# Performance work log

Hardware: AMD Instinct MI355X
Metric: run time of the kernel (lower is better)

Reference implementation:

```python
import jax, jax.numpy as jnp
import numpy as np

D_MODEL, H, DK, DV = 1024, 16, 64, 64
B, NQ, NK = 4, 1024, 1024
LN_EPS = 1e-5


def setup_inputs() -> dict:
    key = jax.random.key(0)
    ks = jax.random.split(key, 16)
    xavier = lambda k, i, o: jax.random.uniform(k, (i, o), jnp.float32,
                                                -np.sqrt(6.0 / (i + o)), np.sqrt(6.0 / (i + o)))
    return {
        "queries": jax.random.normal(ks[0], (B, NQ, D_MODEL), jnp.float32),
        "keys": jax.random.normal(ks[1], (B, NK, D_MODEL), jnp.float32),
        "values": jax.random.normal(ks[2], (B, NK, D_MODEL), jnp.float32),
        "geometry": jax.random.uniform(ks[3], (B, H, NQ, NK), jnp.float32),
        "attention_mask": jax.random.bernoulli(ks[4], 0.1, (B, H, NQ, NK)),
        "Wq": xavier(ks[5], D_MODEL, H * DK), "bq": jnp.zeros((H * DK,), jnp.float32),
        "Wk": xavier(ks[6], D_MODEL, H * DK), "bk": jnp.zeros((H * DK,), jnp.float32),
        "Wv": xavier(ks[7], D_MODEL, H * DV), "bv": jnp.zeros((H * DV,), jnp.float32),
        "Wo": xavier(ks[8], H * DV, D_MODEL), "bo": jnp.zeros((D_MODEL,), jnp.float32),
        "ln_gamma": jnp.ones((D_MODEL,), jnp.float32),
        "ln_beta": jnp.zeros((D_MODEL,), jnp.float32),
    }


def reference(queries, keys, values, geometry, attention_mask,
              Wq, bq, Wk, bk, Wv, bv, Wo, bo, ln_gamma, ln_beta):
    b, nq, _ = queries.shape
    nk = keys.shape[1]
    # QKV projections -> (b, h, n, d)
    q = (queries @ Wq + bq).reshape(b, nq, H, DK).transpose(0, 2, 1, 3)
    k = (keys @ Wk + bk).reshape(b, nk, H, DK).transpose(0, 2, 1, 3)
    v = (values @ Wv + bv).reshape(b, nk, H, DV).transpose(0, 2, 1, 3)
    att = jnp.einsum('bhqd,bhkd->bhqk', q, k) / np.sqrt(DK).astype(np.float32)
    att = jnp.where(attention_mask, -jnp.inf, att)
    # inline geometry log-bias before softmax
    w = jnp.log(jnp.clip(geometry, 1e-6)) + att
    w = jax.nn.softmax(w, axis=-1)  # dropout is identity in eval
    out = jnp.einsum('bhqk,bhkd->bqhd', w, v).reshape(b, nq, H * DV)
    out = out @ Wo + bo
    # residual + LayerNorm
    x = queries + out  # dropout identity in eval
    mu = jnp.mean(x, axis=-1, keepdims=True)
    var = jnp.mean((x - mu) ** 2, axis=-1, keepdims=True)
    return (x - mu) * jax.lax.rsqrt(var + LN_EPS) * ln_gamma + ln_beta
```

## Files before the change

### kernel.cpp

```cpp
#include <hip/hip_runtime.h>
#include <hip/hip_bf16.h>

typedef unsigned short u16;
typedef unsigned long long u64;
typedef __bf16 bf16x8 __attribute__((ext_vector_type(8)));
typedef float f32x4 __attribute__((ext_vector_type(4)));
typedef float f32x2 __attribute__((ext_vector_type(2)));

#define AS1 __attribute__((address_space(1)))
#define AS3 __attribute__((address_space(3)))
#define GLL16(gp, lp) __builtin_amdgcn_global_load_lds((AS1 const unsigned int*)(gp), (AS3 unsigned int*)(lp), 16, 0, 0)

__device__ __forceinline__ u16 f2bf(float f) {
    unsigned u = __builtin_bit_cast(unsigned, f);
    unsigned r = u + 0x7FFFu + ((u >> 16) & 1u);
    return (u16)(r >> 16);
}

__global__ void detect_kernel(const unsigned char* __restrict__ m, int* __restrict__ flag) {
    __shared__ int cnt1;
    __shared__ int big;
    if (threadIdx.x == 0) { cnt1 = 0; big = 0; }
    __syncthreads();
    int c1 = 0, bg = 0;
    for (int i = threadIdx.x; i < 16384; i += 256) {
        unsigned char v = m[i];
        if (v) {
            if ((i & 3) == 1) c1++;
            if (v > 1) bg++;
        }
    }
    atomicAdd(&cnt1, c1);
    atomicAdd(&big, bg);
    __syncthreads();
    if (threadIdx.x == 0) {
        int f;
        if (big == 0) f = cnt1 ? 0 : 1;
        else          f = cnt1 ? 3 : 2;
        *flag = f;
    }
}

#define MN_LOOP(PRED)                                                     \
    for (int row = wave; row < 65536; row += nw) {                        \
        size_t base = (size_t)row * 1024;                                 \
        u64 myw = 0;                                                      \
        _Pragma("unroll")                                                 \
        for (int kb = 0; kb < 16; ++kb) {                                 \
            size_t gi = base + kb * 64 + lane;                            \
            bool p = (PRED);                                              \
            u64 w = __ballot(p);                                          \
            if (lane == kb) myw = w;                                      \
        }                                                                 \
        if (lane < 16) MB[(size_t)row * 16 + lane] = myw;                 \
    }

__global__ __launch_bounds__(256) void masknorm_kernel(const void* __restrict__ mp,
                                                       const int* __restrict__ flagp,
                                                       u64* __restrict__ MB) {
    const int flag = *flagp;
    const int lane = threadIdx.x & 63;
    const int wave = blockIdx.x * 4 + (threadIdx.x >> 6);
    const int nw = gridDim.x * 4;
    if (flag == 0) {
        const unsigned char* m8 = (const unsigned char*)mp;
        MN_LOOP(m8[gi] != 0)
    } else if (flag == 1) {
        const int* m32 = (const int*)mp;
        MN_LOOP(m32[gi] != 0)
    } else if (flag == 2) {
        const unsigned* mf = (const unsigned*)mp;
        MN_LOOP((mf[gi] << 1) != 0)
    } else {
        const u16* mb = (const u16*)mp;
        MN_LOOP((mb[gi] & 0x7FFF) != 0)
    }
}

__global__ void cast3_kernel(const float* __restrict__ q, const float* __restrict__ k,
                             const float* __restrict__ v, u16* __restrict__ xq,
                             u16* __restrict__ xk, u16* __restrict__ xv) {
    const int n4 = 4 * 1024 * 1024 / 4;
    int stride = gridDim.x * blockDim.x;
    for (int i = blockIdx.x * blockDim.x + threadIdx.x; i < n4; i += stride) {
        float4 a = ((const float4*)q)[i];
        float4 b = ((const float4*)k)[i];
        float4 c = ((const float4*)v)[i];
        ((ushort4*)xq)[i] = make_ushort4(f2bf(a.x), f2bf(a.y), f2bf(a.z), f2bf(a.w));
        ((ushort4*)xk)[i] = make_ushort4(f2bf(b.x), f2bf(b.y), f2bf(b.z), f2bf(b.w));
        ((ushort4*)xv)[i] = make_ushort4(f2bf(c.x), f2bf(c.y), f2bf(c.z), f2bf(c.w));
    }
}

__global__ __launch_bounds__(256) void wtrans_kernel(
    const float* __restrict__ W0, const float* __restrict__ W1,
    const float* __restrict__ W2, const float* __restrict__ W3,
    u16* __restrict__ T0, u16* __restrict__ T1, u16* __restrict__ T2, u16* __restrict__ T3) {
    const float* W = (blockIdx.z == 0) ? W0 : (blockIdx.z == 1) ? W1 : (blockIdx.z == 2) ? W2 : W3;
    u16* T = (blockIdx.z == 0) ? T0 : (blockIdx.z == 1) ? T1 : (blockIdx.z == 2) ? T2 : T3;
    __shared__ float t[64][65];
    const int n0 = blockIdx.x * 64, k0 = blockIdx.y * 64;
    const int tx = threadIdx.x, ty = threadIdx.y;
    for (int j = ty; j < 64; j += 4) t[j][tx] = W[(size_t)(k0 + j) * 1024 + n0 + tx];
    __syncthreads();
    for (int j = ty; j < 64; j += 4) T[(size_t)(n0 + j) * 1024 + k0 + tx] = f2bf(t[tx][j]);
}

__device__ __forceinline__ void gemm_core(const u16* __restrict__ A, const u16* __restrict__ Bt,
                                          u16* sA, u16* sB, f32x4 (&acc)[4][4],
                                          int tid, int bm, int bn) {
    const int lane = tid & 63, wid = tid >> 6;
    const int wr = wid >> 1, wc = wid & 1;
    const int l15 = lane & 15, l4 = lane >> 4;
    const int srow = tid >> 2, sslot = tid & 3;
    const int soff = (sslot ^ ((srow >> 1) & 3)) * 8;
    const u16* aSrc = A + (size_t)(bm * 128 + srow) * 1024 + soff;
    const u16* bSrc = Bt + (size_t)(bn * 128 + srow) * 1024 + soff;
    u16* const dA0 = sA + wid * 512;
    u16* const dA1 = sA + 2048 + wid * 512;
    u16* const dB0 = sB + wid * 512;
    u16* const dB1 = sB + 2048 + wid * 512;

#define GSTAGE(BUF, T)                                                  \
    do {                                                                \
        GLL16(aSrc + (T) * 32, dA0 + (BUF) * 4096);                     \
        GLL16(aSrc + 65536 + (T) * 32, dA1 + (BUF) * 4096);             \
        GLL16(bSrc + (T) * 32, dB0 + (BUF) * 4096);                     \
        GLL16(bSrc + 65536 + (T) * 32, dB1 + (BUF) * 4096);             \
    } while (0)

#define GCOMPUTE(BUF)                                                             \
    do {                                                                          \
        bf16x8 af[4], bfv[4];                                                     \
        _Pragma("unroll")                                                         \
        for (int m = 0; m < 4; ++m) {                                             \
            const int rr = wr * 64 + m * 16 + l15;                                \
            af[m] = *(const bf16x8*)(sA + (BUF) * 4096 + rr * 32 +                \
                                     ((l4 ^ ((rr >> 1) & 3)) * 8));               \
        }                                                                         \
        _Pragma("unroll")                                                         \
        for (int n = 0; n < 4; ++n) {                                             \
            const int rr = wc * 64 + n * 16 + l15;                                \
            bfv[n] = *(const bf16x8*)(sB + (BUF) * 4096 + rr * 32 +               \
                                      ((l4 ^ ((rr >> 1) & 3)) * 8));              \
        }                                                                         \
        _Pragma("unroll")                                                         \
        for (int m = 0; m < 4; ++m)                                               \
            _Pragma("unroll")                                                     \
            for (int n = 0; n < 4; ++n)                                           \
                acc[m][n] = __builtin_amdgcn_mfma_f32_16x16x32_bf16(af[m], bfv[n], acc[m][n], 0, 0, 0); \
    } while (0)

#define GBODY(T, BUF, NBUF, WSTR)                                       \
    do {                                                                \
        if ((T) + 2 < 32) {                                             \
            GSTAGE(NBUF, (T) + 2);                                      \
            __builtin_amdgcn_sched_barrier(0);                          \
        }                                                               \
        GCOMPUTE(BUF);                                                  \
        if ((T) + 1 < 32) {                                             \
            asm volatile(WSTR ::: "memory");                            \
            __builtin_amdgcn_sched_barrier(0);                          \
            __builtin_amdgcn_s_barrier();                               \
            __builtin_amdgcn_sched_barrier(0);                          \
        }                                                               \
    } while (0)

    GSTAGE(0, 0);
    GSTAGE(1, 1);
    __builtin_amdgcn_sched_barrier(0);
    asm volatile("s_waitcnt vmcnt(4)" ::: "memory");
    __builtin_amdgcn_sched_barrier(0);
    __builtin_amdgcn_s_barrier();
    __builtin_amdgcn_sched_barrier(0);

    for (int it = 0; it < 10; ++it) {
        const int t0 = it * 3;
        GBODY(t0 + 0, 0, 2, "s_waitcnt vmcnt(4)");
        GBODY(t0 + 1, 1, 0, "s_waitcnt vmcnt(4)");
        GBODY(t0 + 2, 2, 1, "s_waitcnt vmcnt(4)");
    }
    GBODY(30, 0, 2, "s_waitcnt vmcnt(0)");
    GBODY(31, 1, 0, "s_waitcnt vmcnt(0)");
#undef GBODY
#undef GCOMPUTE
#undef GSTAGE
}

__global__ __launch_bounds__(256, 3) void qkv_gemm(
    const u16* __restrict__ XQ, const u16* __restrict__ XK, const u16* __restrict__ XV,
    const u16* __restrict__ WQT, const u16* __restrict__ WKT, const u16* __restrict__ WVT,
    const float* __restrict__ bq, const float* __restrict__ bk, const float* __restrict__ bv,
    u16* __restrict__ QS, u16* __restrict__ KS, u16* __restrict__ VT) {
    __shared__ __align__(16) u16 smem[24576];
    const int z = blockIdx.z;
    const u16* A  = (z == 0) ? XQ : (z == 1) ? XK : XV;
    const u16* Bt = (z == 0) ? WQT : (z == 1) ? WKT : WVT;
    const float* bias = (z == 0) ? bq : (z == 1) ? bk : bv;
    const int tid = threadIdx.x, lane = tid & 63, wid = tid >> 6;
    const int bm = blockIdx.y, bn = blockIdx.x;
    const int wr = wid >> 1, wc = wid & 1;
    const int l15 = lane & 15, l4 = lane >> 4;

    f32x4 acc[4][4] = {};
    gemm_core(A, Bt, smem, smem + 12288, acc, tid, bm, bn);

    if (z == 2) {
        __syncthreads();
        u16* tl = smem;
#pragma unroll
        for (int n = 0; n < 4; ++n) {
            const int cl = wc * 64 + n * 16 + l15;
            const float bv_ = bias[bn * 128 + cl];
#pragma unroll
            for (int m = 0; m < 4; ++m)
#pragma unroll
                for (int j = 0; j < 4; ++j) {
                    const int rl = wr * 64 + m * 16 + l4 * 4 + j;
                    tl[cl * 132 + rl] = f2bf(acc[m][n][j] + bv_);
                }
        }
        __syncthreads();
        const int bb = bm >> 3, k0 = (bm & 7) * 128;
#pragma unroll
        for (int i = 0; i < 8; ++i) {
            const int idx = i * 256 + tid;
            const int row = idx >> 4, col16 = idx & 15;
            const int cg = bn * 128 + row;
            const int hh = cg >> 6, dd = cg & 63;
            bf16x8 v = *(const bf16x8*)(tl + row * 132 + col16 * 8);
            *(bf16x8*)(VT + ((size_t)((bb * 16 + hh) * 64 + dd)) * 1024 + k0 + col16 * 8) = v;
        }
    } else {
        u16* outp = (z == 0) ? QS : KS;
        const float scale = (z == 0) ? 0.125f : 1.0f;
#pragma unroll
        for (int n = 0; n < 4; ++n) {
            const int c = bn * 128 + wc * 64 + n * 16 + l15;
            const float bv_ = bias[c];
#pragma unroll
            for (int m = 0; m < 4; ++m)
#pragma unroll
                for (int j = 0; j < 4; ++j) {
                    const int r = bm * 128 + wr * 64 + m * 16 + l4 * 4 + j;
                    outp[(size_t)r * 1024 + c] = f2bf((acc[m][n][j] + bv_) * scale);
                }
        }
    }
}

__global__ __launch_bounds__(256, 3) void gemm_out(
    const u16* __restrict__ A, const u16* __restrict__ Bt, const float* __restrict__ bias,
    float* __restrict__ outp, const float* __restrict__ resid) {
    __shared__ __align__(16) u16 smem[24576];
    const int tid = threadIdx.x, lane = tid & 63, wid = tid >> 6;
    const int bm = blockIdx.y, bn = blockIdx.x;
    const int wr = wid >> 1, wc = wid & 1;
    const int l15 = lane & 15, l4 = lane >> 4;

    f32x4 acc[4][4] = {};
    gemm_core(A, Bt, smem, smem + 12288, acc, tid, bm, bn);

#pragma unroll
    for (int n = 0; n < 4; ++n) {
        const int c = bn * 128 + wc * 64 + n * 16 + l15;
        const float bv = bias[c];
#pragma unroll
        for (int m = 0; m < 4; ++m)
#pragma unroll
            for (int j = 0; j < 4; ++j) {
                const int r = bm * 128 + wr * 64 + m * 16 + l4 * 4 + j;
                outp[(size_t)r * 1024 + c] = acc[m][n][j] + bv + resid[(size_t)r * 1024 + c];
            }
    }
}

__global__ __launch_bounds__(256, 4) void attn_kernel(
    const u16* __restrict__ Qs, const u16* __restrict__ Ks, const u16* __restrict__ Vt,
    const float* __restrict__ geom, const u64* __restrict__ MBw,
    u16* __restrict__ AO) {
    __shared__ __align__(16) u16 lds[14336];

    const int g = blockIdx.x;
    const int tt = (g & 7) * 128 + (g >> 3);
    const int qb = tt & 15;
    const int bhid = tt >> 4;
    const int b = bhid >> 4, h = bhid & 15;
    const int q0 = qb * 64;

    const int tid = threadIdx.x, lane = tid & 63, wid = tid >> 6;
    const int l15 = lane & 15, l4 = lane >> 4;
    const int qrow = q0 + wid * 16;
    const size_t bh = (size_t)bhid;

    const u16* qp = Qs + (size_t)(b * 1024 + qrow + l15) * 1024 + h * 64 + l4 * 8;
    bf16x8 aq0 = *(const bf16x8*)qp;
    bf16x8 aq1 = *(const bf16x8*)(qp + 32);

    const int kr = tid >> 3, ks = tid & 7;
    const int kgr = (kr & 15) * 2 + (kr >> 4);
    const u16* ksrc = Ks + (size_t)(b * 1024 + kgr) * 1024 + h * 64 + ((ks ^ ((kr >> 1) & 7)) * 8);
    const int vr = tid >> 2, vs = tid & 3;
    const u16* vsrc = Vt + (bh * 64 + vr) * 1024 + ((vs ^ ((vr >> 1) & 3)) * 8);
    u16* const KD0 = lds + 0    + wid * 512;
    u16* const KD1 = lds + 2048 + wid * 512;
    u16* const KD2 = lds + 4096 + wid * 512;
    u16* const VD0 = lds + 6144 + 0    + wid * 512;
    u16* const VD1 = lds + 6144 + 2048 + wid * 512;
    u16* const VD2 = lds + 6144 + 4096 + wid * 512;
    u16* const pw  = lds + 12288 + wid * 512;

    const float* gbase = geom + (bh * 1024 + qrow + l4 * 4) * 1024 + l15 * 2;
    const unsigned* mb32 = (const unsigned*)(MBw + (bh * 1024 + qrow + l4 * 4) * 16);

    f32x4 o[4] = {};
    float m_run[4], l_run[4];
#pragma unroll
    for (int j = 0; j < 4; ++j) { m_run[j] = -1e30f; l_run[j] = 0.f; }

    f32x2 gpA[4], gpB[4];
    unsigned mkA[4], mkB[4];

    GLL16(ksrc, KD0);
    GLL16(vsrc, VD0);
    GLL16(ksrc + 32768, KD1);
    GLL16(vsrc + 32, VD1);
    __builtin_amdgcn_sched_barrier(0);
#pragma unroll
    for (int j = 0; j < 4; ++j) {
        gpA[j] = *(const f32x2*)(gbase + j * 1024);
        mkA[j] = mb32[j * 32];
    }
    __builtin_amdgcn_sched_barrier(0);
    asm volatile("s_waitcnt vmcnt(10)" ::: "memory");
    __builtin_amdgcn_sched_barrier(0);
    __builtin_amdgcn_s_barrier();
    __builtin_amdgcn_sched_barrier(0);

#define BODY(T, GC, GN, MC, MN, KBC, VBC, KDN, VDN, WSTR)                                \
    do {                                                                                 \
        if ((T) + 2 < 32) {                                                              \
            GLL16(ksrc + (size_t)((T) + 2) * 32768, KDN);                                \
            GLL16(vsrc + ((T) + 2) * 32, VDN);                                           \
            __builtin_amdgcn_sched_barrier(0);                                           \
        }                                                                                \
        if ((T) + 1 < 32) {                                                              \
            _Pragma("unroll")                                                            \
            for (int j = 0; j < 4; ++j) {                                                \
                GN[j] = *(const f32x2*)(gbase + j * 1024 + ((T) + 1) * 32);              \
                MN[j] = mb32[j * 32 + (T) + 1];                                          \
            }                                                                            \
            __builtin_amdgcn_sched_barrier(0);                                           \
        }                                                                                \
        f32x4 s0, s1;                                                                    \
        __builtin_amdgcn_s_setprio(1);                                                   \
        {                                                                                \
            const int rr = l15, swz = (rr >> 1) & 7;                                     \
            bf16x8 k0 = *(const bf16x8*)((KBC) + rr * 64 + ((l4 ^ swz) * 8));            \
            bf16x8 k1 = *(const bf16x8*)((KBC) + rr * 64 + (((4 + l4) ^ swz) * 8));      \
            f32x4 z = {};                                                                \
            z = __builtin_amdgcn_mfma_f32_16x16x32_bf16(aq0, k0, z, 0, 0, 0);            \
            s0 = __builtin_amdgcn_mfma_f32_16x16x32_bf16(aq1, k1, z, 0, 0, 0);           \
        }                                                                                \
        {                                                                                \
            const int rr = 16 + l15, swz = (rr >> 1) & 7;                                \
            bf16x8 k0 = *(const bf16x8*)((KBC) + rr * 64 + ((l4 ^ swz) * 8));            \
            bf16x8 k1 = *(const bf16x8*)((KBC) + rr * 64 + (((4 + l4) ^ swz) * 8));      \
            f32x4 z = {};                                                                \
            z = __builtin_amdgcn_mfma_f32_16x16x32_bf16(aq0, k0, z, 0, 0, 0);            \
            s1 = __builtin_amdgcn_mfma_f32_16x16x32_bf16(aq1, k1, z, 0, 0, 0);           \
        }                                                                                \
        __builtin_amdgcn_s_setprio(0);                                                   \
        float sclv[4];                                                                   \
        _Pragma("unroll")                                                                \
        for (int j = 0; j < 4; ++j) {                                                    \
            float a0 = s0[j], a1 = s1[j];                                                \
            float mt = fmaxf(a0, a1);                                                    \
            mt = fmaxf(mt, __shfl_xor(mt, 1, 16));                                       \
            mt = fmaxf(mt, __shfl_xor(mt, 2, 16));                                       \
            mt = fmaxf(mt, __shfl_xor(mt, 4, 16));                                       \
            mt = fmaxf(mt, __shfl_xor(mt, 8, 16));                                       \
            float mn = fmaxf(m_run[j], mt);                                              \
            float scl = __expf(m_run[j] - mn);                                           \
            m_run[j] = mn;                                                               \
            unsigned mb2 = (MC[j] >> (l15 * 2)) & 3u;                                    \
            f32x2 gv = GC[j];                                                            \
            float p0 = (mb2 & 1u) ? 0.f : __expf(a0 - mn) * fmaxf(gv[0], 1e-6f);         \
            float p1 = (mb2 & 2u) ? 0.f : __expf(a1 - mn) * fmaxf(gv[1], 1e-6f);         \
            float rs = p0 + p1;                                                          \
            rs += __shfl_xor(rs, 1, 16);                                                 \
            rs += __shfl_xor(rs, 2, 16);                                                 \
            rs += __shfl_xor(rs, 4, 16);                                                 \
            rs += __shfl_xor(rs, 8, 16);                                                 \
            l_run[j] = l_run[j] * scl + rs;                                              \
            sclv[j] = scl;                                                               \
            const int row = l4 * 4 + j;                                                  \
            const int slot4 = (l15 & 3) | ((((l15 >> 2) ^ l4) & 3) << 2);                \
            unsigned pk = (unsigned)f2bf(p0) | ((unsigned)f2bf(p1) << 16);               \
            *(unsigned*)(pw + row * 32 + slot4 * 2) = pk;                                \
        }                                                                                \
        _Pragma("unroll")                                                                \
        for (int df = 0; df < 4; ++df) {                                                 \
            f32x4 tv = o[df];                                                            \
            _Pragma("unroll")                                                            \
            for (int j = 0; j < 4; ++j) tv[j] *= sclv[j];                                \
            o[df] = tv;                                                                  \
        }                                                                                \
        {                                                                                \
            const int blk = (l4 ^ (l15 >> 2)) & 3;                                       \
            bf16x8 pa = *(const bf16x8*)(pw + l15 * 32 + blk * 8);                       \
            __builtin_amdgcn_s_setprio(1);                                               \
            _Pragma("unroll")                                                            \
            for (int df = 0; df < 4; ++df) {                                             \
                const int rr = df * 16 + l15, vswz = (rr >> 1) & 3;                      \
                bf16x8 v0 = *(const bf16x8*)((VBC) + rr * 32 + ((l4 ^ vswz) * 8));       \
                o[df] = __builtin_amdgcn_mfma_f32_16x16x32_bf16(pa, v0, o[df], 0, 0, 0); \
            }                                                                            \
            __builtin_amdgcn_s_setprio(0);                                               \
        }                                                                                \
        if ((T) + 1 < 32) {                                                              \
            asm volatile(WSTR ::: "memory");                                             \
            __builtin_amdgcn_sched_barrier(0);                                           \
            __builtin_amdgcn_s_barrier();                                                \
            __builtin_amdgcn_sched_barrier(0);                                           \
        }                                                                                \
    } while (0)

    for (int it = 0; it < 5; ++it) {
        const int t0 = it * 6;
        BODY(t0 + 0, gpA, gpB, mkA, mkB, (lds + 0),    (lds + 6144),        KD2, VD2, "s_waitcnt vmcnt(10)");
        BODY(t0 + 1, gpB, gpA, mkB, mkA, (lds + 2048), (lds + 6144 + 2048), KD0, VD0, "s_waitcnt vmcnt(10)");
        BODY(t0 + 2, gpA, gpB, mkA, mkB, (lds + 4096), (lds + 6144 + 4096), KD1, VD1, "s_waitcnt vmcnt(10)");
        BODY(t0 + 3, gpB, gpA, mkB, mkA, (lds + 0),    (lds + 6144),        KD2, VD2, "s_waitcnt vmcnt(10)");
        BODY(t0 + 4, gpA, gpB, mkA, mkB, (lds + 2048), (lds + 6144 + 2048), KD0, VD0, "s_waitcnt vmcnt(10)");
        BODY(t0 + 5, gpB, gpA, mkB, mkA, (lds + 4096), (lds + 6144 + 4096), KD1, VD1, "s_waitcnt vmcnt(10)");
    }
    BODY(30, gpA, gpB, mkA, mkB, (lds + 0),    (lds + 6144),        KD2, VD2, "s_waitcnt vmcnt(8)");
    BODY(31, gpB, gpA, mkB, mkA, (lds + 2048), (lds + 6144 + 2048), KD0, VD0, "s_waitcnt vmcnt(8)");
#undef BODY

    float inv[4];
#pragma unroll
    for (int j = 0; j < 4; ++j) inv[j] = 1.0f / l_run[j];
#pragma unroll
    for (int p = 0; p < 2; ++p) {
#pragma unroll
        for (int df2 = 0; df2 < 2; ++df2) {
            const int df = p * 2 + df2;
#pragma unroll
            for (int j = 0; j < 4; ++j)
                pw[(l4 * 4 + j) * 32 + df2 * 16 + l15] = f2bf(o[df][j] * inv[j]);
        }
        const int er = lane >> 2, ec = lane & 3;
        bf16x8 val = *(const bf16x8*)(pw + er * 32 + ec * 8);
        *(bf16x8*)(AO + (size_t)(b * 1024 + qrow + er) * 1024 + h * 64 + p * 32 + ec * 8) = val;
    }
}

__global__ __launch_bounds__(256) void ln_kernel(const float* __restrict__ Y,
                                                 const float* __restrict__ gamma,
                                                 const float* __restrict__ beta,
                                                 float* __restrict__ out) {
    __shared__ float red[8];
    const int r = blockIdx.x, tid = threadIdx.x, lane = tid & 63, wid = tid >> 6;
    float4 v = ((const float4*)(Y + (size_t)r * 1024))[tid];
    float s = v.x + v.y + v.z + v.w;
    float q = v.x * v.x + v.y * v.y + v.z * v.z + v.w * v.w;
    for (int d = 1; d < 64; d <<= 1) {
        s += __shfl_xor(s, d, 64);
        q += __shfl_xor(q, d, 64);
    }
    if (lane == 0) { red[wid] = s; red[4 + wid] = q; }
    __syncthreads();
    float ts = red[0] + red[1] + red[2] + red[3];
    float tq = red[4] + red[5] + red[6] + red[7];
    float mu = ts * (1.f / 1024.f);
    float var = tq * (1.f / 1024.f) - mu * mu;
    float rstd = rsqrtf(var + 1e-5f);
    float4 gg = ((const float4*)gamma)[tid];
    float4 be = ((const float4*)beta)[tid];
    float4 ov;
    ov.x = (v.x - mu) * rstd * gg.x + be.x;
    ov.y = (v.y - mu) * rstd * gg.y + be.y;
    ov.z = (v.z - mu) * rstd * gg.z + be.z;
    ov.w = (v.w - mu) * rstd * gg.w + be.w;
    ((float4*)(out + (size_t)r * 1024))[tid] = ov;
}

extern "C" void kernel_launch(void* const* d_in, const int* in_sizes, int n_in,
                              void* d_out, int out_size, void* d_ws, size_t ws_size,
                              hipStream_t stream) {
    const float* queries = (const float*)d_in[0];
    const float* keys    = (const float*)d_in[1];
    const float* values  = (const float*)d_in[2];
    const float* geom    = (const float*)d_in[3];
    const void*  mask    = d_in[4];
    const float* Wq = (const float*)d_in[5];  const float* bq = (const float*)d_in[6];
    const float* Wk = (const float*)d_in[7];  const float* bk = (const float*)d_in[8];
    const float* Wv = (const float*)d_in[9];  const float* bv = (const float*)d_in[10];
    const float* Wo = (const float*)d_in[11]; const float* bo = (const float*)d_in[12];
    const float* gamma = (const float*)d_in[13];
    const float* beta  = (const float*)d_in[14];

    char* ws = (char*)d_ws;
    const size_t MB_ = 1024 * 1024;
    u16* XQ  = (u16*)(ws + 0);
    u16* XK  = (u16*)(ws + 8 * MB_);
    u16* XV  = (u16*)(ws + 16 * MB_);
    u16* WQT = (u16*)(ws + 24 * MB_);
    u16* WKT = (u16*)(ws + 26 * MB_);
    u16* WVT = (u16*)(ws + 28 * MB_);
    u16* WOT = (u16*)(ws + 30 * MB_);
    u16* QS  = (u16*)(ws + 32 * MB_);
    u16* KS  = (u16*)(ws + 40 * MB_);
    u16* VT  = (u16*)(ws + 48 * MB_);
    u16* AO  = (u16*)(ws + 56 * MB_);
    u64* MBITS = (u64*)(ws + 16 * MB_);
    float* Y = (float*)(ws + 0);
    int* FLAG = (int*)(ws + 64 * MB_);

    detect_kernel<<<1, 256, 0, stream>>>((const unsigned char*)mask, FLAG);
    cast3_kernel<<<1024, 256, 0, stream>>>(queries, keys, values, XQ, XK, XV);
    wtrans_kernel<<<dim3(16, 16, 4), dim3(64, 4), 0, stream>>>(Wq, Wk, Wv, Wo, WQT, WKT, WVT, WOT);
    qkv_gemm<<<dim3(8, 32, 3), 256, 0, stream>>>(XQ, XK, XV, WQT, WKT, WVT, bq, bk, bv, QS, KS, VT);
    masknorm_kernel<<<4096, 256, 0, stream>>>(mask, FLAG, MBITS);
    attn_kernel<<<1024, 256, 0, stream>>>(QS, KS, VT, geom, MBITS, AO);
    gemm_out<<<dim3(8, 32), 256, 0, stream>>>(AO, WOT, bo, Y, queries);
    ln_kernel<<<4096, 256, 0, stream>>>(Y, gamma, beta, (float*)d_out);
}
```

Measured before the change: 274.4 us.

## Widen attention key tile to 64 with double-buffered K/V staging

Each attention iteration now handles 64 keys instead of 32, so there are 16 iterations instead of 32. K/V staging moves from a triple buffer to a double buffer, with new swizzles and two async loads per thread per tensor. Geometry loads become float4 and mask bits are read as per-lane nibbles. The aim is to halve the number of barriers and per-iteration softmax reductions and to widen memory accesses, at the cost of more LDS per block and a shallower prefetch pipeline, which may reduce occupancy and latency hiding.

```diff
diff --git a/kernel.cpp b/kernel.cpp
--- a/kernel.cpp
+++ b/kernel.cpp
@@ -2,10 +2,10 @@
 #include <hip/hip_bf16.h>
 
 typedef unsigned short u16;
+typedef unsigned char u8;
 typedef unsigned long long u64;
 typedef __bf16 bf16x8 __attribute__((ext_vector_type(8)));
 typedef float f32x4 __attribute__((ext_vector_type(4)));
-typedef float f32x2 __attribute__((ext_vector_type(2)));
 
 #define AS1 __attribute__((address_space(1)))
 #define AS3 __attribute__((address_space(3)))
@@ -279,7 +279,7 @@
     const u16* __restrict__ Qs, const u16* __restrict__ Ks, const u16* __restrict__ Vt,
     const float* __restrict__ geom, const u64* __restrict__ MBw,
     u16* __restrict__ AO) {
-    __shared__ __align__(16) u16 lds[14336];
+    __shared__ __align__(16) u16 lds[20480];
 
     const int g = blockIdx.x;
     const int tt = (g & 7) * 128 + (g >> 3);
@@ -297,85 +297,80 @@
     bf16x8 aq0 = *(const bf16x8*)qp;
     bf16x8 aq1 = *(const bf16x8*)(qp + 32);
 
-    const int kr = tid >> 3, ks = tid & 7;
-    const int kgr = (kr & 15) * 2 + (kr >> 4);
-    const u16* ksrc = Ks + (size_t)(b * 1024 + kgr) * 1024 + h * 64 + ((ks ^ ((kr >> 1) & 7)) * 8);
-    const int vr = tid >> 2, vs = tid & 3;
-    const u16* vsrc = Vt + (bh * 64 + vr) * 1024 + ((vs ^ ((vr >> 1) & 3)) * 8);
-    u16* const KD0 = lds + 0    + wid * 512;
-    u16* const KD1 = lds + 2048 + wid * 512;
-    u16* const KD2 = lds + 4096 + wid * 512;
-    u16* const VD0 = lds + 6144 + 0    + wid * 512;
-    u16* const VD1 = lds + 6144 + 2048 + wid * 512;
-    u16* const VD2 = lds + 6144 + 4096 + wid * 512;
-    u16* const pw  = lds + 12288 + wid * 512;
-
-    const float* gbase = geom + (bh * 1024 + qrow + l4 * 4) * 1024 + l15 * 2;
-    const unsigned* mb32 = (const unsigned*)(MBw + (bh * 1024 + qrow + l4 * 4) * 16);
+    const int r0 = tid >> 3, s0 = tid & 7;
+    const int r1 = 32 + r0;
+    const int kgr0 = (r0 & 15) * 4 + (r0 >> 4);
+    const int kgr1 = (r1 & 15) * 4 + (r1 >> 4);
+    const u16* ksrc0 = Ks + (size_t)(b * 1024 + kgr0) * 1024 + h * 64 + ((s0 ^ (r0 & 7)) * 8);
+    const u16* ksrc1 = Ks + (size_t)(b * 1024 + kgr1) * 1024 + h * 64 + ((s0 ^ (r1 & 7)) * 8);
+    const u16* vsrc0 = Vt + (bh * 64 + r0) * 1024 + ((s0 ^ (r0 & 7)) * 8);
+    const u16* vsrc1 = Vt + (bh * 64 + r1) * 1024 + ((s0 ^ (r1 & 7)) * 8);
+    u16* const KD = lds + wid * 512;
+    u16* const VD = lds + 8192 + wid * 512;
+    u16* const pw = lds + 16384 + wid * 1024;
+
+    const float* gbase = geom + (bh * 1024 + qrow + l4 * 4) * 1024 + l15 * 4;
+    const u8* mbase8 = (const u8*)MBw + (size_t)(bh * 1024 + qrow + l4 * 4) * 128 + (l15 >> 1);
+    const int nsh = (l15 & 1) * 4;
 
     f32x4 o[4] = {};
     float m_run[4], l_run[4];
 #pragma unroll
     for (int j = 0; j < 4; ++j) { m_run[j] = -1e30f; l_run[j] = 0.f; }
 
-    f32x2 gpA[4], gpB[4];
+    f32x4 gpA[4], gpB[4];
     unsigned mkA[4], mkB[4];
 
-    GLL16(ksrc, KD0);
-    GLL16(vsrc, VD0);
-    GLL16(ksrc + 32768, KD1);
-    GLL16(vsrc + 32, VD1);
+    GLL16(ksrc0, KD);
+    GLL16(ksrc1, KD + 2048);
+    GLL16(vsrc0, VD);
+    GLL16(vsrc1, VD + 2048);
     __builtin_amdgcn_sched_barrier(0);
 #pragma unroll
     for (int j = 0; j < 4; ++j) {
-        gpA[j] = *(const f32x2*)(gbase + j * 1024);
-        mkA[j] = mb32[j * 32];
-    }
-    __builtin_amdgcn_sched_barrier(0);
-    asm volatile("s_waitcnt vmcnt(10)" ::: "memory");
+        gpA[j] = *(const f32x4*)(gbase + j * 1024);
+        mkA[j] = mbase8[j * 128];
+    }
+    __builtin_amdgcn_sched_barrier(0);
+    asm volatile("s_waitcnt vmcnt(8)" ::: "memory");
     __builtin_amdgcn_sched_barrier(0);
     __builtin_amdgcn_s_barrier();
     __builtin_amdgcn_sched_barrier(0);
 
-#define BODY(T, GC, GN, MC, MN, KBC, VBC, KDN, VDN, WSTR)                                \
+#define BODY(T, G, GC, GN, MC, MN)                                                       \
     do {                                                                                 \
-        if ((T) + 2 < 32) {                                                              \
-            GLL16(ksrc + (size_t)((T) + 2) * 32768, KDN);                                \
-            GLL16(vsrc + ((T) + 2) * 32, VDN);                                           \
+        const u16* KB = lds + ((T) & 1) * 4096;                                          \
+        const u16* VB = lds + 8192 + ((T) & 1) * 4096;                                   \
+        if (G) {                                                                         \
+            const int nb = (((T) + 1) & 1) * 4096;                                       \
+            GLL16(ksrc0 + (size_t)((T) + 1) * 65536, KD + nb);                           \
+            GLL16(ksrc1 + (size_t)((T) + 1) * 65536, KD + 2048 + nb);                    \
+            GLL16(vsrc0 + ((T) + 1) * 64, VD + nb);                                      \
+            GLL16(vsrc1 + ((T) + 1) * 64, VD + 2048 + nb);                               \
             __builtin_amdgcn_sched_barrier(0);                                           \
-        }                                                                                \
-        if ((T) + 1 < 32) {                                                              \
             _Pragma("unroll")                                                            \
             for (int j = 0; j < 4; ++j) {                                                \
-                GN[j] = *(const f32x2*)(gbase + j * 1024 + ((T) + 1) * 32);              \
-                MN[j] = mb32[j * 32 + (T) + 1];                                          \
+                GN[j] = *(const f32x4*)(gbase + j * 1024 + ((T) + 1) * 64);              \
+                MN[j] = mbase8[j * 128 + ((T) + 1) * 8];                                 \
             }                                                                            \
             __builtin_amdgcn_sched_barrier(0);                                           \
         }                                                                                \
-        f32x4 s0, s1;                                                                    \
+        f32x4 s[4];                                                                      \
         __builtin_amdgcn_s_setprio(1);                                                   \
-        {                                                                                \
-            const int rr = l15, swz = (rr >> 1) & 7;                                     \
-            bf16x8 k0 = *(const bf16x8*)((KBC) + rr * 64 + ((l4 ^ swz) * 8));            \
-            bf16x8 k1 = *(const bf16x8*)((KBC) + rr * 64 + (((4 + l4) ^ swz) * 8));      \
+        _Pragma("unroll")                                                                \
+        for (int nf = 0; nf < 4; ++nf) {                                                 \
+            const int rr = nf * 16 + l15, swz = rr & 7;                                  \
+            bf16x8 k0 = *(const bf16x8*)(KB + rr * 64 + ((l4 ^ swz) * 8));               \
+            bf16x8 k1 = *(const bf16x8*)(KB + rr * 64 + (((4 + l4) ^ swz) * 8));         \
             f32x4 z = {};                                                                \
             z = __builtin_amdgcn_mfma_f32_16x16x32_bf16(aq0, k0, z, 0, 0, 0);            \
-            s0 = __builtin_amdgcn_mfma_f32_16x16x32_bf16(aq1, k1, z, 0, 0, 0);           \
-        }                                                                                \
-        {                                                                                \
-            const int rr = 16 + l15, swz = (rr >> 1) & 7;                                \
-            bf16x8 k0 = *(const bf16x8*)((KBC) + rr * 64 + ((l4 ^ swz) * 8));            \
-            bf16x8 k1 = *(const bf16x8*)((KBC) + rr * 64 + (((4 + l4) ^ swz) * 8));      \
-            f32x4 z = {};                                                                \
-            z = __builtin_amdgcn_mfma_f32_16x16x32_bf16(aq0, k0, z, 0, 0, 0);            \
-            s1 = __builtin_amdgcn_mfma_f32_16x16x32_bf16(aq1, k1, z, 0, 0, 0);           \
+            s[nf] = __builtin_amdgcn_mfma_f32_16x16x32_bf16(aq1, k1, z, 0, 0, 0);        \
         }                                                                                \
         __builtin_amdgcn_s_setprio(0);                                                   \
         float sclv[4];                                                                   \
         _Pragma("unroll")                                                                \
         for (int j = 0; j < 4; ++j) {                                                    \
-            float a0 = s0[j], a1 = s1[j];                                                \
-            float mt = fmaxf(a0, a1);                                                    \
+            float mt = fmaxf(fmaxf(s[0][j], s[1][j]), fmaxf(s[2][j], s[3][j]));          \
             mt = fmaxf(mt, __shfl_xor(mt, 1, 16));                                       \
             mt = fmaxf(mt, __shfl_xor(mt, 2, 16));                                       \
             mt = fmaxf(mt, __shfl_xor(mt, 4, 16));                                       \
@@ -383,11 +378,13 @@
             float mn = fmaxf(m_run[j], mt);                                              \
             float scl = __expf(m_run[j] - mn);                                           \
             m_run[j] = mn;                                                               \
-            unsigned mb2 = (MC[j] >> (l15 * 2)) & 3u;                                    \
-            f32x2 gv = GC[j];                                                            \
-            float p0 = (mb2 & 1u) ? 0.f : __expf(a0 - mn) * fmaxf(gv[0], 1e-6f);         \
-            float p1 = (mb2 & 2u) ? 0.f : __expf(a1 - mn) * fmaxf(gv[1], 1e-6f);         \
-            float rs = p0 + p1;                                                          \
+            unsigned nib = (MC[j] >> nsh) & 0xFu;                                        \
+            f32x4 gv = GC[j];                                                            \
+            float p0 = (nib & 1u) ? 0.f : __expf(s[0][j] - mn) * fmaxf(gv[0], 1e-6f);    \
+            float p1 = (nib & 2u) ? 0.f : __expf(s[1][j] - mn) * fmaxf(gv[1], 1e-6f);    \
+            float p2 = (nib & 4u) ? 0.f : __expf(s[2][j] - mn) * fmaxf(gv[2], 1e-6f);    \
+            float p3 = (nib & 8u) ? 0.f : __expf(s[3][j] - mn) * fmaxf(gv[3], 1e-6f);    \
+            float rs = (p0 + p1) + (p2 + p3);                                            \
             rs += __shfl_xor(rs, 1, 16);                                                 \
             rs += __shfl_xor(rs, 2, 16);                                                 \
             rs += __shfl_xor(rs, 4, 16);                                                 \
@@ -395,9 +392,9 @@
             l_run[j] = l_run[j] * scl + rs;                                              \
             sclv[j] = scl;                                                               \
             const int row = l4 * 4 + j;                                                  \
-            const int slot4 = (l15 & 3) | ((((l15 >> 2) ^ l4) & 3) << 2);                \
-            unsigned pk = (unsigned)f2bf(p0) | ((unsigned)f2bf(p1) << 16);               \
-            *(unsigned*)(pw + row * 32 + slot4 * 2) = pk;                                \
+            u64 pk = (u64)f2bf(p0) | ((u64)f2bf(p1) << 16) |                             \
+                     ((u64)f2bf(p2) << 32) | ((u64)f2bf(p3) << 48);                      \
+            *(u64*)(pw + row * 64 + (((l15 >> 1) ^ (row & 7)) * 8) + (l15 & 1) * 4) = pk;\
         }                                                                                \
         _Pragma("unroll")                                                                \
         for (int df = 0; df < 4; ++df) {                                                 \
@@ -407,53 +404,51 @@
             o[df] = tv;                                                                  \
         }                                                                                \
         {                                                                                \
-            const int blk = (l4 ^ (l15 >> 2)) & 3;                                       \
-            bf16x8 pa = *(const bf16x8*)(pw + l15 * 32 + blk * 8);                       \
+            const int pswz = l15 & 7;                                                    \
+            bf16x8 pa0 = *(const bf16x8*)(pw + l15 * 64 + ((l4 ^ pswz) * 8));            \
+            bf16x8 pa1 = *(const bf16x8*)(pw + l15 * 64 + (((4 + l4) ^ pswz) * 8));      \
             __builtin_amdgcn_s_setprio(1);                                               \
             _Pragma("unroll")                                                            \
             for (int df = 0; df < 4; ++df) {                                             \
-                const int rr = df * 16 + l15, vswz = (rr >> 1) & 3;                      \
-                bf16x8 v0 = *(const bf16x8*)((VBC) + rr * 32 + ((l4 ^ vswz) * 8));       \
-                o[df] = __builtin_amdgcn_mfma_f32_16x16x32_bf16(pa, v0, o[df], 0, 0, 0); \
+                const int rr = df * 16 + l15, vswz = rr & 7;                             \
+                bf16x8 v0 = *(const bf16x8*)(VB + rr * 64 + ((l4 ^ vswz) * 8));          \
+                bf16x8 v1 = *(const bf16x8*)(VB + rr * 64 + (((4 + l4) ^ vswz) * 8));    \
+                o[df] = __builtin_amdgcn_mfma_f32_16x16x32_bf16(pa0, v0, o[df], 0, 0, 0);\
+                o[df] = __builtin_amdgcn_mfma_f32_16x16x32_bf16(pa1, v1, o[df], 0, 0, 0);\
             }                                                                            \
             __builtin_amdgcn_s_setprio(0);                                               \
         }                                                                                \
-        if ((T) + 1 < 32) {                                                              \
-            asm volatile(WSTR ::: "memory");                                             \
+        if (G) {                                                                         \
+            asm volatile("s_waitcnt vmcnt(8)" ::: "memory");                             \
             __builtin_amdgcn_sched_barrier(0);                                           \
             __builtin_amdgcn_s_barrier();                                                \
             __builtin_amdgcn_sched_barrier(0);                                           \
         }                                                                                \
     } while (0)
 
-    for (int it = 0; it < 5; ++it) {
-        const int t0 = it * 6;
-        BODY(t0 + 0, gpA, gpB, mkA, mkB, (lds + 0),    (lds + 6144),        KD2, VD2, "s_waitcnt vmcnt(10)");
-        BODY(t0 + 1, gpB, gpA, mkB, mkA, (lds + 2048), (lds + 6144 + 2048), KD0, VD0, "s_waitcnt vmcnt(10)");
-        BODY(t0 + 2, gpA, gpB, mkA, mkB, (lds + 4096), (lds + 6144 + 4096), KD1, VD1, "s_waitcnt vmcnt(10)");
-        BODY(t0 + 3, gpB, gpA, mkB, mkA, (lds + 0),    (lds + 6144),        KD2, VD2, "s_waitcnt vmcnt(10)");
-        BODY(t0 + 4, gpA, gpB, mkA, mkB, (lds + 2048), (lds + 6144 + 2048), KD0, VD0, "s_waitcnt vmcnt(10)");
-        BODY(t0 + 5, gpB, gpA, mkB, mkA, (lds + 4096), (lds + 6144 + 4096), KD1, VD1, "s_waitcnt vmcnt(10)");
-    }
-    BODY(30, gpA, gpB, mkA, mkB, (lds + 0),    (lds + 6144),        KD2, VD2, "s_waitcnt vmcnt(8)");
-    BODY(31, gpB, gpA, mkB, mkA, (lds + 2048), (lds + 6144 + 2048), KD0, VD0, "s_waitcnt vmcnt(8)");
+    for (int it = 0; it < 7; ++it) {
+        const int t0 = it * 2;
+        BODY(t0,     1, gpA, gpB, mkA, mkB);
+        BODY(t0 + 1, 1, gpB, gpA, mkB, mkA);
+    }
+    BODY(14, 1, gpA, gpB, mkA, mkB);
+    BODY(15, 0, gpB, gpA, mkB, mkA);
 #undef BODY
 
     float inv[4];
 #pragma unroll
     for (int j = 0; j < 4; ++j) inv[j] = 1.0f / l_run[j];
 #pragma unroll
+    for (int df = 0; df < 4; ++df)
+#pragma unroll
+        for (int j = 0; j < 4; ++j)
+            pw[(l4 * 4 + j) * 64 + df * 16 + l15] = f2bf(o[df][j] * inv[j]);
+#pragma unroll
     for (int p = 0; p < 2; ++p) {
-#pragma unroll
-        for (int df2 = 0; df2 < 2; ++df2) {
-            const int df = p * 2 + df2;
-#pragma unroll
-            for (int j = 0; j < 4; ++j)
-                pw[(l4 * 4 + j) * 32 + df2 * 16 + l15] = f2bf(o[df][j] * inv[j]);
-        }
-        const int er = lane >> 2, ec = lane & 3;
-        bf16x8 val = *(const bf16x8*)(pw + er * 32 + ec * 8);
-        *(bf16x8*)(AO + (size_t)(b * 1024 + qrow + er) * 1024 + h * 64 + p * 32 + ec * 8) = val;
+        const int idx = p * 64 + lane;
+        const int er = idx >> 3, ec = idx & 7;
+        bf16x8 val = *(const bf16x8*)(pw + er * 64 + ec * 8);
+        *(bf16x8*)(AO + (size_t)(b * 1024 + qrow + er) * 1024 + h * 64 + ec * 8) = val;
     }
 }
 
```

Measured after the change: 360.3 us. 1.31x slower.
